# Performance work log

Hardware: AMD Instinct MI355X
Metric: run time of the kernel (lower is better)

## Reference

```python
import jax, jax.numpy as jnp
import numpy as np

SQ, B, NP, HN = 2048, 2, 16, 64  # [seq, batch, heads, head_dim]

def setup_inputs() -> dict:
    key = jax.random.key(0)
    kq, kk, kv = jax.random.split(key, 3)
    return {
        "query": jax.random.normal(kq, (SQ, B, NP, HN), dtype=jnp.float32),
        "key":   jax.random.normal(kk, (SQ, B, NP, HN), dtype=jnp.float32),
        "value": jax.random.normal(kv, (SQ, B, NP, HN), dtype=jnp.float32),
    }

def reference(query, key, value):
    sq, b, nheads, hn = query.shape
    # NOTE: original module computes norm_factor=sqrt(hn) but never applies it;
    # scores are UNscaled QK^T, replicated faithfully here.
    scores = jnp.einsum('sbnh,tbnh->bnst', query, key)          # [b, np, sq, sk]
    probs = jax.nn.softmax(scores, axis=-1)                      # mask=None -> plain softmax
    # dropout is deterministic (train=False default) -> identity
    context = jnp.einsum('bnst,tbnh->sbnh', probs, value)        # [sq, b, np, hn]
    return context.reshape(sq, b, nheads * hn).astype(jnp.float32)
```

## Files before the change

### kernel.cpp

```cpp
#include <hip/hip_runtime.h>
#include <math.h>

#define SQ 2048
#define NBH 32
#define HN 64
#define BQ 128
#define BK 64
#define TOK 2048
#define LDK 72

typedef _Float16 half2v __attribute__((ext_vector_type(2)));
typedef _Float16 half4v __attribute__((ext_vector_type(4)));
typedef _Float16 half8v __attribute__((ext_vector_type(8)));
typedef float f32x16 __attribute__((ext_vector_type(16)));

__global__ __launch_bounds__(256, 3)
void fattn_mfma(const float* __restrict__ Q, const float* __restrict__ K,
                const float* __restrict__ V, float* __restrict__ O) {
  __shared__ __align__(16) _Float16 kb[BK][LDK];
  __shared__ __align__(16) _Float16 vt[HN][LDK];

  const int t = threadIdx.x;
  const int lane = t & 63;
  const int w = t >> 6;
  const int h2 = lane >> 5;
  const int l31 = lane & 31;
  const int q0 = blockIdx.x * BQ + w * 32;
  const size_t hoff = (size_t)blockIdx.y * HN;

  half8v qf[4];
  {
    const float* qp = Q + (size_t)(q0 + l31) * TOK + hoff + 8 * h2;
    #pragma unroll
    for (int ks = 0; ks < 4; ++ks) {
      float4 a = *(const float4*)(qp + 16 * ks);
      float4 b = *(const float4*)(qp + 16 * ks + 4);
      half8v f;
      f[0] = (_Float16)a.x; f[1] = (_Float16)a.y; f[2] = (_Float16)a.z; f[3] = (_Float16)a.w;
      f[4] = (_Float16)b.x; f[5] = (_Float16)b.y; f[6] = (_Float16)b.z; f[7] = (_Float16)b.w;
      qf[ks] = f;
    }
  }

  f32x16 acc0, acc1;
  #pragma unroll
  for (int r = 0; r < 16; ++r) { acc0[r] = 0.f; acc1[r] = 0.f; }
  float m_i = -INFINITY, l_i = 0.f;

  for (int kt = 0; kt < SQ; kt += BK) {
    __syncthreads();
    {
      const int key = t >> 2, qq = t & 3;
      const float* kp = K + (size_t)(kt + key) * TOK + hoff;
      #pragma unroll
      for (int i = 0; i < 4; ++i) {
        const int d = qq * 4 + i * 16;
        float4 x = *(const float4*)(kp + d);
        half4v h;
        h[0] = (_Float16)x.x; h[1] = (_Float16)x.y; h[2] = (_Float16)x.z; h[3] = (_Float16)x.w;
        *(half4v*)&kb[key][d] = h;
      }
    }
    {
      const int kp2 = (t >> 3) * 2;
      const int m = t & 7;
      const int db = m * 8;
      const float* v0 = V + (size_t)(kt + kp2) * TOK + hoff + db;
      const float* v1 = v0 + TOK;
      float4 a0 = *(const float4*)v0;
      float4 a1 = *(const float4*)(v0 + 4);
      float4 b0 = *(const float4*)v1;
      float4 b1 = *(const float4*)(v1 + 4);
      float av[8] = {a0.x, a0.y, a0.z, a0.w, a1.x, a1.y, a1.z, a1.w};
      float bv[8] = {b0.x, b0.y, b0.z, b0.w, b1.x, b1.y, b1.z, b1.w};
      const int keyS = kp2 ^ (m << 3);
      #pragma unroll
      for (int j = 0; j < 8; ++j) {
        half2v h; h[0] = (_Float16)av[j]; h[1] = (_Float16)bv[j];
        *(half2v*)&vt[db + j][keyS] = h;
      }
    }
    __syncthreads();

    f32x16 sf0, sf1;
    {
      f32x16 c0, c1;
      #pragma unroll
      for (int r = 0; r < 16; ++r) { c0[r] = 0.f; c1[r] = 0.f; }
      #pragma unroll
      for (int ks = 0; ks < 4; ++ks) {
        half8v a0v = *(const half8v*)&kb[l31][8 * h2 + 16 * ks];
        half8v a1v = *(const half8v*)&kb[l31 + 32][8 * h2 + 16 * ks];
        c0 = __builtin_amdgcn_mfma_f32_32x32x16_f16(a0v, qf[ks], c0, 0, 0, 0);
        c1 = __builtin_amdgcn_mfma_f32_32x32x16_f16(a1v, qf[ks], c1, 0, 0, 0);
      }
      sf0 = c0; sf1 = c1;
    }

    float mx = -INFINITY;
    #pragma unroll
    for (int r = 0; r < 16; ++r) mx = fmaxf(mx, fmaxf(sf0[r], sf1[r]));
    mx = fmaxf(mx, __shfl_xor(mx, 32, 64));
    const float mnew = fmaxf(m_i, mx);
    const float alpha = __expf(m_i - mnew);
    float rsum = 0.f;
    #pragma unroll
    for (int r = 0; r < 16; ++r) {
      float p0 = __expf(sf0[r] - mnew);
      float p1 = __expf(sf1[r] - mnew);
      sf0[r] = p0; sf1[r] = p1;
      rsum += p0 + p1;
    }
    rsum += __shfl_xor(rsum, 32, 64);
    l_i = l_i * alpha + rsum;
    m_i = mnew;
    #pragma unroll
    for (int r = 0; r < 16; ++r) { acc0[r] *= alpha; acc1[r] *= alpha; }

    #pragma unroll
    for (int ks = 0; ks < 4; ++ks) {
      const int rb = 8 * (ks & 1);
      const f32x16& s = (ks < 2) ? sf0 : sf1;
      union { half8v v8; half2v v2[4]; } pu;
      #pragma unroll
      for (int tt = 0; tt < 4; ++tt) {
        auto pk = __builtin_amdgcn_cvt_pkrtz(s[rb + 2 * tt], s[rb + 2 * tt + 1]);
        pu.v2[tt] = *(half2v*)&pk;
      }
      #pragma unroll
      for (int mbd = 0; mbd < 2; ++mbd) {
        const int dim = l31 + 32 * mbd;
        const int swz = (dim >> 3) & 7;
        union { half8v v8; half4v v4[2]; } au;
        au.v4[0] = *(const half4v*)&vt[dim][(((2 * ks)     ^ swz) * 8) + 4 * h2];
        au.v4[1] = *(const half4v*)&vt[dim][(((2 * ks + 1) ^ swz) * 8) + 4 * h2];
        if (mbd == 0)
          acc0 = __builtin_amdgcn_mfma_f32_32x32x16_f16(au.v8, pu.v8, acc0, 0, 0, 0);
        else
          acc1 = __builtin_amdgcn_mfma_f32_32x32x16_f16(au.v8, pu.v8, acc1, 0, 0, 0);
      }
    }
  }

  const float invl = 1.f / l_i;
  float* orow = O + (size_t)(q0 + l31) * TOK + hoff;
  #pragma unroll
  for (int r = 0; r < 16; ++r) {
    const int d = (r & 3) + 8 * (r >> 2) + 4 * h2;
    orow[d]      = acc0[r] * invl;
    orow[d + 32] = acc1[r] * invl;
  }
}

extern "C" void kernel_launch(void* const* d_in, const int* in_sizes, int n_in,
                              void* d_out, int out_size, void* d_ws, size_t ws_size,
                              hipStream_t stream) {
  const float* Q = (const float*)d_in[0];
  const float* K = (const float*)d_in[1];
  const float* V = (const float*)d_in[2];
  float* O = (float*)d_out;
  dim3 grid(SQ / BQ, NBH);
  dim3 block(256);
  fattn_mfma<<<grid, block, 0, stream>>>(Q, K, V, O);
}
```

Before: 153.0 us.

## Double-buffer K/V tiles with register prefetch of the next tile

Prefetches the next K and V tile from global memory into registers before computing on the current tile, then converts it and writes it into a second shared-memory buffer after the compute. The goal is to hide global load latency behind the MFMA and softmax work. In exchange, shared memory doubles, registers grow by 32 floats per thread (which may reduce occupancy under launch_bounds 256,3), and each iteration still keeps two barriers.

Result: slower. 162.8 us (+6.4%).

```diff
diff --git a/kernel.cpp b/kernel.cpp
--- a/kernel.cpp
+++ b/kernel.cpp
@@ -6,6 +6,7 @@
 #define HN 64
 #define BQ 128
 #define BK 64
+#define NT (SQ/BK)
 #define TOK 2048
 #define LDK 72
 
@@ -14,11 +15,53 @@
 typedef _Float16 half8v __attribute__((ext_vector_type(8)));
 typedef float f32x16 __attribute__((ext_vector_type(16)));
 
+
+__device__ __forceinline__
+void load_stage(const float* __restrict__ K, const float* __restrict__ V,
+                int kt, size_t hoff, int t, float4 kr[4], float4 vr[4]) {
+  const int key = t >> 2, qq = t & 3;
+  const float* kp = K + (size_t)(kt + key) * TOK + hoff;
+  #pragma unroll
+  for (int i = 0; i < 4; ++i)
+    kr[i] = *(const float4*)(kp + qq * 4 + i * 16);
+  const int kp2 = (t >> 3) * 2, m = t & 7, db = m * 8;
+  const float* v0 = V + (size_t)(kt + kp2) * TOK + hoff + db;
+  vr[0] = *(const float4*)v0;
+  vr[1] = *(const float4*)(v0 + 4);
+  vr[2] = *(const float4*)(v0 + TOK);
+  vr[3] = *(const float4*)(v0 + TOK + 4);
+}
+
+__device__ __forceinline__
+void write_stage(_Float16 (*kb)[LDK], _Float16 (*vt)[LDK], int t,
+                 const float4 kr[4], const float4 vr[4]) {
+  const int key = t >> 2, qq = t & 3;
+  #pragma unroll
+  for (int i = 0; i < 4; ++i) {
+    const int d = qq * 4 + i * 16;
+    half4v h;
+    h[0] = (_Float16)kr[i].x; h[1] = (_Float16)kr[i].y;
+    h[2] = (_Float16)kr[i].z; h[3] = (_Float16)kr[i].w;
+    *(half4v*)&kb[key][d] = h;
+  }
+  const int kp2 = (t >> 3) * 2, m = t & 7, db = m * 8;
+  const int keyS = kp2 ^ (m << 3);
+  const float av[8] = {vr[0].x, vr[0].y, vr[0].z, vr[0].w,
+                       vr[1].x, vr[1].y, vr[1].z, vr[1].w};
+  const float bv[8] = {vr[2].x, vr[2].y, vr[2].z, vr[2].w,
+                       vr[3].x, vr[3].y, vr[3].z, vr[3].w};
+  #pragma unroll
+  for (int j = 0; j < 8; ++j) {
+    half2v h; h[0] = (_Float16)av[j]; h[1] = (_Float16)bv[j];
+    *(half2v*)&vt[db + j][keyS] = h;
+  }
+}
+
 __global__ __launch_bounds__(256, 3)
 void fattn_mfma(const float* __restrict__ Q, const float* __restrict__ K,
                 const float* __restrict__ V, float* __restrict__ O) {
-  __shared__ __align__(16) _Float16 kb[BK][LDK];
-  __shared__ __align__(16) _Float16 vt[HN][LDK];
+  __shared__ __align__(16) _Float16 kb[2][BK][LDK];
+  __shared__ __align__(16) _Float16 vt[2][HN][LDK];
 
   const int t = threadIdx.x;
   const int lane = t & 63;
@@ -47,40 +90,15 @@
   for (int r = 0; r < 16; ++r) { acc0[r] = 0.f; acc1[r] = 0.f; }
   float m_i = -INFINITY, l_i = 0.f;
 
-  for (int kt = 0; kt < SQ; kt += BK) {
-    __syncthreads();
-    {
-      const int key = t >> 2, qq = t & 3;
-      const float* kp = K + (size_t)(kt + key) * TOK + hoff;
-      #pragma unroll
-      for (int i = 0; i < 4; ++i) {
-        const int d = qq * 4 + i * 16;
-        float4 x = *(const float4*)(kp + d);
-        half4v h;
-        h[0] = (_Float16)x.x; h[1] = (_Float16)x.y; h[2] = (_Float16)x.z; h[3] = (_Float16)x.w;
-        *(half4v*)&kb[key][d] = h;
-      }
-    }
-    {
-      const int kp2 = (t >> 3) * 2;
-      const int m = t & 7;
-      const int db = m * 8;
-      const float* v0 = V + (size_t)(kt + kp2) * TOK + hoff + db;
-      const float* v1 = v0 + TOK;
-      float4 a0 = *(const float4*)v0;
-      float4 a1 = *(const float4*)(v0 + 4);
-      float4 b0 = *(const float4*)v1;
-      float4 b1 = *(const float4*)(v1 + 4);
-      float av[8] = {a0.x, a0.y, a0.z, a0.w, a1.x, a1.y, a1.z, a1.w};
-      float bv[8] = {b0.x, b0.y, b0.z, b0.w, b1.x, b1.y, b1.z, b1.w};
-      const int keyS = kp2 ^ (m << 3);
-      #pragma unroll
-      for (int j = 0; j < 8; ++j) {
-        half2v h; h[0] = (_Float16)av[j]; h[1] = (_Float16)bv[j];
-        *(half2v*)&vt[db + j][keyS] = h;
-      }
-    }
-    __syncthreads();
+  float4 kr[4], vr[4];
+  load_stage(K, V, 0, hoff, t, kr, vr);
+  write_stage(kb[0], vt[0], t, kr, vr);
+  __syncthreads();
+
+  for (int it = 0; it < NT; ++it) {
+    const int cur = it & 1;
+    if (it + 1 < NT)
+      load_stage(K, V, (it + 1) * BK, hoff, t, kr, vr);
 
     f32x16 sf0, sf1;
     {
@@ -89,8 +107,8 @@
       for (int r = 0; r < 16; ++r) { c0[r] = 0.f; c1[r] = 0.f; }
       #pragma unroll
       for (int ks = 0; ks < 4; ++ks) {
-        half8v a0v = *(const half8v*)&kb[l31][8 * h2 + 16 * ks];
-        half8v a1v = *(const half8v*)&kb[l31 + 32][8 * h2 + 16 * ks];
+        half8v a0v = *(const half8v*)&kb[cur][l31][8 * h2 + 16 * ks];
+        half8v a1v = *(const half8v*)&kb[cur][l31 + 32][8 * h2 + 16 * ks];
         c0 = __builtin_amdgcn_mfma_f32_32x32x16_f16(a0v, qf[ks], c0, 0, 0, 0);
         c1 = __builtin_amdgcn_mfma_f32_32x32x16_f16(a1v, qf[ks], c1, 0, 0, 0);
       }
@@ -132,13 +150,19 @@
         const int dim = l31 + 32 * mbd;
         const int swz = (dim >> 3) & 7;
         union { half8v v8; half4v v4[2]; } au;
-        au.v4[0] = *(const half4v*)&vt[dim][(((2 * ks)     ^ swz) * 8) + 4 * h2];
-        au.v4[1] = *(const half4v*)&vt[dim][(((2 * ks + 1) ^ swz) * 8) + 4 * h2];
+        au.v4[0] = *(const half4v*)&vt[cur][dim][(((2 * ks)     ^ swz) * 8) + 4 * h2];
+        au.v4[1] = *(const half4v*)&vt[cur][dim][(((2 * ks + 1) ^ swz) * 8) + 4 * h2];
         if (mbd == 0)
           acc0 = __builtin_amdgcn_mfma_f32_32x32x16_f16(au.v8, pu.v8, acc0, 0, 0, 0);
         else
           acc1 = __builtin_amdgcn_mfma_f32_32x32x16_f16(au.v8, pu.v8, acc1, 0, 0, 0);
       }
+    }
+
+    if (it + 1 < NT) {
+      __syncthreads();
+      write_stage(kb[cur ^ 1], vt[cur ^ 1], t, kr, vr);
+      __syncthreads();
     }
   }
 
```

## Halve query tile to 64 with 128-thread blocks and widen K/V staging loads

Applied to the files above, without the earlier changes.

Shrinks each block to two waves covering 64 query rows, which doubles the grid to 1024 blocks and fills more CUs. The K/V staging loop is reworked so each thread loads twice as much: K rows are split in halves and written as 8-wide fp16 vectors, and V is transposed four keys at a time with 4-wide stores. The cost is that K/V tiles are re-read from global memory twice as often per query row, and each block has less parallelism to hide load latency.

New measurement: 201.5 us. 31.7% more time.

```diff
diff --git a/kernel.cpp b/kernel.cpp
--- a/kernel.cpp
+++ b/kernel.cpp
@@ -4,8 +4,9 @@
 #define SQ 2048
 #define NBH 32
 #define HN 64
-#define BQ 128
+#define BQ 64
 #define BK 64
+#define NT (SQ/BK)
 #define TOK 2048
 #define LDK 72
 
@@ -14,7 +15,7 @@
 typedef _Float16 half8v __attribute__((ext_vector_type(8)));
 typedef float f32x16 __attribute__((ext_vector_type(16)));
 
-__global__ __launch_bounds__(256, 3)
+__global__ __launch_bounds__(128, 2)
 void fattn_mfma(const float* __restrict__ Q, const float* __restrict__ K,
                 const float* __restrict__ V, float* __restrict__ O) {
   __shared__ __align__(16) _Float16 kb[BK][LDK];
@@ -27,6 +28,13 @@
   const int l31 = lane & 31;
   const int q0 = blockIdx.x * BQ + w * 32;
   const size_t hoff = (size_t)blockIdx.y * HN;
+
+  const int skey = t >> 1;
+  const int shalf = t & 1;
+  const int vm = t & 7;
+  const int vdb = vm * 8;
+  const int vkp = (t >> 3) * 4;
+  const int vkeyS = vkp ^ (vm << 3);
 
   half8v qf[4];
   {
@@ -50,34 +58,38 @@
   for (int kt = 0; kt < SQ; kt += BK) {
     __syncthreads();
     {
-      const int key = t >> 2, qq = t & 3;
-      const float* kp = K + (size_t)(kt + key) * TOK + hoff;
+      const float* kp = K + (size_t)(kt + skey) * TOK + hoff + shalf * 32;
       #pragma unroll
       for (int i = 0; i < 4; ++i) {
-        const int d = qq * 4 + i * 16;
-        float4 x = *(const float4*)(kp + d);
-        half4v h;
-        h[0] = (_Float16)x.x; h[1] = (_Float16)x.y; h[2] = (_Float16)x.z; h[3] = (_Float16)x.w;
-        *(half4v*)&kb[key][d] = h;
+        float4 a = *(const float4*)(kp + i * 8);
+        float4 b = *(const float4*)(kp + i * 8 + 4);
+        half8v h;
+        h[0] = (_Float16)a.x; h[1] = (_Float16)a.y; h[2] = (_Float16)a.z; h[3] = (_Float16)a.w;
+        h[4] = (_Float16)b.x; h[5] = (_Float16)b.y; h[6] = (_Float16)b.z; h[7] = (_Float16)b.w;
+        *(half8v*)&kb[skey][shalf * 32 + i * 8] = h;
       }
     }
     {
-      const int kp2 = (t >> 3) * 2;
-      const int m = t & 7;
-      const int db = m * 8;
-      const float* v0 = V + (size_t)(kt + kp2) * TOK + hoff + db;
-      const float* v1 = v0 + TOK;
-      float4 a0 = *(const float4*)v0;
-      float4 a1 = *(const float4*)(v0 + 4);
-      float4 b0 = *(const float4*)v1;
-      float4 b1 = *(const float4*)(v1 + 4);
-      float av[8] = {a0.x, a0.y, a0.z, a0.w, a1.x, a1.y, a1.z, a1.w};
-      float bv[8] = {b0.x, b0.y, b0.z, b0.w, b1.x, b1.y, b1.z, b1.w};
-      const int keyS = kp2 ^ (m << 3);
+      const float* v0 = V + (size_t)(kt + vkp) * TOK + hoff + vdb;
+      float4 r0a = *(const float4*)v0;
+      float4 r0b = *(const float4*)(v0 + 4);
+      float4 r1a = *(const float4*)(v0 + TOK);
+      float4 r1b = *(const float4*)(v0 + TOK + 4);
+      float4 r2a = *(const float4*)(v0 + 2 * TOK);
+      float4 r2b = *(const float4*)(v0 + 2 * TOK + 4);
+      float4 r3a = *(const float4*)(v0 + 3 * TOK);
+      float4 r3b = *(const float4*)(v0 + 3 * TOK + 4);
+      const float rv[4][8] = {
+        {r0a.x, r0a.y, r0a.z, r0a.w, r0b.x, r0b.y, r0b.z, r0b.w},
+        {r1a.x, r1a.y, r1a.z, r1a.w, r1b.x, r1b.y, r1b.z, r1b.w},
+        {r2a.x, r2a.y, r2a.z, r2a.w, r2b.x, r2b.y, r2b.z, r2b.w},
+        {r3a.x, r3a.y, r3a.z, r3a.w, r3b.x, r3b.y, r3b.z, r3b.w}};
       #pragma unroll
       for (int j = 0; j < 8; ++j) {
-        half2v h; h[0] = (_Float16)av[j]; h[1] = (_Float16)bv[j];
-        *(half2v*)&vt[db + j][keyS] = h;
+        half4v h;
+        h[0] = (_Float16)rv[0][j]; h[1] = (_Float16)rv[1][j];
+        h[2] = (_Float16)rv[2][j]; h[3] = (_Float16)rv[3][j];
+        *(half4v*)&vt[vdb + j][vkeyS] = h;
       }
     }
     __syncthreads();
@@ -160,6 +172,6 @@
   const float* V = (const float*)d_in[2];
   float* O = (float*)d_out;
   dim3 grid(SQ / BQ, NBH);
-  dim3 block(256);
+  dim3 block(128);
   fattn_mfma<<<grid, block, 0, stream>>>(Q, K, V, O);
 }
```

## Pre-convert K/V to fp16 swizzled layout and double-buffer tiles via async LDS loads

Applied to the files above, without the earlier changes.

Adds two prep kernels that convert K to fp16 with an XOR-swizzled row layout and V to a transposed fp16 layout in workspace. The attention kernel then streams the tiles into double-buffered shared memory with global_load_lds, so the next tile loads while the current one computes, and each iteration needs only one barrier. This removes the per-block fp32 loads and conversions that were repeated across 16 query blocks and halves the bytes read per tile. In exchange it adds two extra launches and a workspace round trip, doubles shared memory use, and lowers the occupancy hint from 3 to 2 blocks.

Result: slower. 159.7 us (+4.4%).

```diff
diff --git a/kernel.cpp b/kernel.cpp
--- a/kernel.cpp
+++ b/kernel.cpp
@@ -1,24 +1,85 @@
 #include <hip/hip_runtime.h>
 #include <math.h>
+#include <stdint.h>
 
 #define SQ 2048
 #define NBH 32
 #define HN 64
 #define BQ 128
 #define BK 64
+#define NT (SQ/BK)
 #define TOK 2048
-#define LDK 72
+#define HSTRIDE (SQ*HN)
 
 typedef _Float16 half2v __attribute__((ext_vector_type(2)));
 typedef _Float16 half4v __attribute__((ext_vector_type(4)));
 typedef _Float16 half8v __attribute__((ext_vector_type(8)));
 typedef float f32x16 __attribute__((ext_vector_type(16)));
 
-__global__ __launch_bounds__(256, 3)
-void fattn_mfma(const float* __restrict__ Q, const float* __restrict__ K,
-                const float* __restrict__ V, float* __restrict__ O) {
-  __shared__ __align__(16) _Float16 kb[BK][LDK];
-  __shared__ __align__(16) _Float16 vt[HN][LDK];
+__device__ __forceinline__ void async16(const void* g, void* l) {
+  __builtin_amdgcn_global_load_lds(
+      (const __attribute__((address_space(1))) void*)g,
+      (__attribute__((address_space(3))) void*)l, 16, 0, 0);
+}
+
+__global__ __launch_bounds__(256) void prep_k(const float* __restrict__ K,
+                                              _Float16* __restrict__ Kh) {
+  const int t = threadIdx.x;
+  const int head = blockIdx.y;
+  const int key = blockIdx.x * 64 + (t >> 2);
+  const int c0 = (t & 3) * 2;
+  const float* src = K + (size_t)key * TOK + head * HN + c0 * 8;
+  float4 a = *(const float4*)src;
+  float4 b = *(const float4*)(src + 4);
+  float4 c = *(const float4*)(src + 8);
+  float4 d = *(const float4*)(src + 12);
+  half8v h0, h1;
+  h0[0]=(_Float16)a.x; h0[1]=(_Float16)a.y; h0[2]=(_Float16)a.z; h0[3]=(_Float16)a.w;
+  h0[4]=(_Float16)b.x; h0[5]=(_Float16)b.y; h0[6]=(_Float16)b.z; h0[7]=(_Float16)b.w;
+  h1[0]=(_Float16)c.x; h1[1]=(_Float16)c.y; h1[2]=(_Float16)c.z; h1[3]=(_Float16)c.w;
+  h1[4]=(_Float16)d.x; h1[5]=(_Float16)d.y; h1[6]=(_Float16)d.z; h1[7]=(_Float16)d.w;
+  _Float16* row = Kh + (size_t)head * HSTRIDE + (size_t)key * 64;
+  *(half8v*)&row[((c0    ) ^ (key & 7)) * 8] = h0;
+  *(half8v*)&row[((c0 + 1) ^ (key & 7)) * 8] = h1;
+}
+
+__global__ __launch_bounds__(256) void prep_v(const float* __restrict__ V,
+                                              _Float16* __restrict__ Vt) {
+  __shared__ _Float16 vs[HN * 64];
+  const int t = threadIdx.x;
+  const int head = blockIdx.y;
+  const int kt = blockIdx.x * 64;
+  const int kl = (t >> 3) * 2;
+  const int db = (t & 7) * 8;
+  const float* src = V + (size_t)(kt + kl) * TOK + head * HN + db;
+  float4 a0 = *(const float4*)src;
+  float4 a1 = *(const float4*)(src + 4);
+  float4 b0 = *(const float4*)(src + TOK);
+  float4 b1 = *(const float4*)(src + TOK + 4);
+  const float av[8] = {a0.x,a0.y,a0.z,a0.w,a1.x,a1.y,a1.z,a1.w};
+  const float bv[8] = {b0.x,b0.y,b0.z,b0.w,b1.x,b1.y,b1.z,b1.w};
+  const int u = kl >> 2;
+  #pragma unroll
+  for (int j = 0; j < 8; ++j) {
+    const int dim = db + j;
+    const int pos = u ^ (dim & 15);
+    half2v h; h[0] = (_Float16)av[j]; h[1] = (_Float16)bv[j];
+    *(half2v*)&vs[dim * 64 + pos * 4 + (kl & 3)] = h;
+  }
+  __syncthreads();
+  const int dim = t >> 2;
+  const int q = (t & 3) ^ (dim & 3);
+  const _Float16* srow = &vs[dim * 64 + q * 16];
+  _Float16* drow = Vt + (size_t)head * HSTRIDE + (size_t)dim * SQ + kt + q * 16;
+  *(half8v*)&drow[0] = *(const half8v*)&srow[0];
+  *(half8v*)&drow[8] = *(const half8v*)&srow[8];
+}
+
+__global__ __launch_bounds__(256, 2)
+void fattn_mfma(const float* __restrict__ Q, const _Float16* __restrict__ Kh,
+                const _Float16* __restrict__ Vt, float* __restrict__ O) {
+  __shared__ __align__(16) _Float16 kbf[2][BK * 64];
+  __shared__ __align__(16) _Float16 vtf[2][HN * 64];
 
   const int t = threadIdx.x;
   const int lane = t & 63;
@@ -26,11 +87,13 @@
   const int h2 = lane >> 5;
   const int l31 = lane & 31;
   const int q0 = blockIdx.x * BQ + w * 32;
-  const size_t hoff = (size_t)blockIdx.y * HN;
+  const int head = blockIdx.y;
+  const _Float16* Kp = Kh + (size_t)head * HSTRIDE;
+  const _Float16* Vp = Vt + (size_t)head * HSTRIDE;
 
   half8v qf[4];
   {
-    const float* qp = Q + (size_t)(q0 + l31) * TOK + hoff + 8 * h2;
+    const float* qp = Q + (size_t)(q0 + l31) * TOK + head * HN + 8 * h2;
     #pragma unroll
     for (int ks = 0; ks < 4; ++ks) {
       float4 a = *(const float4*)(qp + 16 * ks);
@@ -47,40 +110,28 @@
   for (int r = 0; r < 16; ++r) { acc0[r] = 0.f; acc1[r] = 0.f; }
   float m_i = -INFINITY, l_i = 0.f;
 
-  for (int kt = 0; kt < SQ; kt += BK) {
+  auto stage = [&](int it) {
+    const int kt = it * BK;
+    const int buf = it & 1;
+    #pragma unroll
+    for (int i = 0; i < 2; ++i) {
+      const int off = w * 1024 + i * 512;
+      async16(Kp + (size_t)kt * 64 + off + lane * 8, &kbf[buf][off]);
+    }
+    #pragma unroll
+    for (int i = 0; i < 2; ++i) {
+      const int off = w * 1024 + i * 512;
+      const int eo = off + lane * 8;
+      const int dim = eo >> 6, inner = eo & 63;
+      async16(Vp + (size_t)dim * SQ + kt + inner, &vtf[buf][off]);
+    }
+  };
+
+  stage(0);
+  for (int it = 0; it < NT; ++it) {
     __syncthreads();
-    {
-      const int key = t >> 2, qq = t & 3;
-      const float* kp = K + (size_t)(kt + key) * TOK + hoff;
-      #pragma unroll
-      for (int i = 0; i < 4; ++i) {
-        const int d = qq * 4 + i * 16;
-        float4 x = *(const float4*)(kp + d);
-        half4v h;
-        h[0] = (_Float16)x.x; h[1] = (_Float16)x.y; h[2] = (_Float16)x.z; h[3] = (_Float16)x.w;
-        *(half4v*)&kb[key][d] = h;
-      }
-    }
-    {
-      const int kp2 = (t >> 3) * 2;
-      const int m = t & 7;
-      const int db = m * 8;
-      const float* v0 = V + (size_t)(kt + kp2) * TOK + hoff + db;
-      const float* v1 = v0 + TOK;
-      float4 a0 = *(const float4*)v0;
-      float4 a1 = *(const float4*)(v0 + 4);
-      float4 b0 = *(const float4*)v1;
-      float4 b1 = *(const float4*)(v1 + 4);
-      float av[8] = {a0.x, a0.y, a0.z, a0.w, a1.x, a1.y, a1.z, a1.w};
-      float bv[8] = {b0.x, b0.y, b0.z, b0.w, b1.x, b1.y, b1.z, b1.w};
-      const int keyS = kp2 ^ (m << 3);
-      #pragma unroll
-      for (int j = 0; j < 8; ++j) {
-        half2v h; h[0] = (_Float16)av[j]; h[1] = (_Float16)bv[j];
-        *(half2v*)&vt[db + j][keyS] = h;
-      }
-    }
-    __syncthreads();
+    if (it + 1 < NT) stage(it + 1);
+    const int cur = it & 1;
 
     f32x16 sf0, sf1;
     {
@@ -89,8 +140,9 @@
       for (int r = 0; r < 16; ++r) { c0[r] = 0.f; c1[r] = 0.f; }
       #pragma unroll
       for (int ks = 0; ks < 4; ++ks) {
-        half8v a0v = *(const half8v*)&kb[l31][8 * h2 + 16 * ks];
-        half8v a1v = *(const half8v*)&kb[l31 + 32][8 * h2 + 16 * ks];
+        const int pos = ((h2 + 2 * ks) ^ (l31 & 7)) * 8;
+        half8v a0v = *(const half8v*)&kbf[cur][l31 * 64 + pos];
+        half8v a1v = *(const half8v*)&kbf[cur][(l31 + 32) * 64 + pos];
         c0 = __builtin_amdgcn_mfma_f32_32x32x16_f16(a0v, qf[ks], c0, 0, 0, 0);
         c1 = __builtin_amdgcn_mfma_f32_32x32x16_f16(a1v, qf[ks], c1, 0, 0, 0);
       }
@@ -130,10 +182,10 @@
       #pragma unroll
       for (int mbd = 0; mbd < 2; ++mbd) {
         const int dim = l31 + 32 * mbd;
-        const int swz = (dim >> 3) & 7;
+        const int sw = dim & 15;
         union { half8v v8; half4v v4[2]; } au;
-        au.v4[0] = *(const half4v*)&vt[dim][(((2 * ks)     ^ swz) * 8) + 4 * h2];
-        au.v4[1] = *(const half4v*)&vt[dim][(((2 * ks + 1) ^ swz) * 8) + 4 * h2];
+        au.v4[0] = *(const half4v*)&vtf[cur][dim * 64 + ((4 * ks + h2)     ^ sw) * 4];
+        au.v4[1] = *(const half4v*)&vtf[cur][dim * 64 + ((4 * ks + 2 + h2) ^ sw) * 4];
         if (mbd == 0)
           acc0 = __builtin_amdgcn_mfma_f32_32x32x16_f16(au.v8, pu.v8, acc0, 0, 0, 0);
         else
@@ -143,7 +195,7 @@
   }
 
   const float invl = 1.f / l_i;
-  float* orow = O + (size_t)(q0 + l31) * TOK + hoff;
+  float* orow = O + (size_t)(q0 + l31) * TOK + head * HN;
   #pragma unroll
   for (int r = 0; r < 16; ++r) {
     const int d = (r & 3) + 8 * (r >> 2) + 4 * h2;
@@ -159,7 +211,9 @@
   const float* K = (const float*)d_in[1];
   const float* V = (const float*)d_in[2];
   float* O = (float*)d_out;
-  dim3 grid(SQ / BQ, NBH);
-  dim3 block(256);
-  fattn_mfma<<<grid, block, 0, stream>>>(Q, K, V, O);
-}
+  _Float16* Kh = (_Float16*)d_ws;
+  _Float16* Vh = Kh + (size_t)NBH * HSTRIDE;
+  prep_k<<<dim3(SQ / 64, NBH), 256, 0, stream>>>(K, Kh);
+  prep_v<<<dim3(SQ / 64, NBH), 256, 0, stream>>>(V, Vh);
+  fattn_mfma<<<dim3(SQ / BQ, NBH), 256, 0, stream>>>(Q, Kh, Vh, O);
+}
```
